# Kernel tuning notes

Hardware: AMD Instinct MI355X
Metric: run time of the kernel (lower is better)

## Reference

```python
import jax, jax.numpy as jnp
import numpy as np

HID = 128
HEADS = 4
N_LAYERS = 3


def layer_norm(x, g, b, eps=1e-5):
    mu = x.mean(-1, keepdims=True)
    var = ((x - mu) ** 2).mean(-1, keepdims=True)
    return (x - mu) / jnp.sqrt(var + eps) * g + b


def gat_layer(x, W, a_src, a_dst, bias, src, dst):
    # PyG GATConv(hidden, hidden, heads=4, concat=False): mean over heads, +bias
    N = x.shape[0]
    z = (x @ W).reshape(N, HEADS, HID)          # [N, H, D]
    e_src = (z * a_src[None]).sum(-1)           # [N, H]
    e_dst = (z * a_dst[None]).sum(-1)           # [N, H]
    e = jax.nn.leaky_relu(e_src[src] + e_dst[dst], 0.2)  # [E, H]
    m = jax.ops.segment_max(e, dst, num_segments=N)
    p = jnp.exp(e - m[dst])
    s = jax.ops.segment_sum(p, dst, num_segments=N)
    w = p / s[dst]                              # softmax over incoming edges
    out = jax.ops.segment_sum(w[:, :, None] * z[src], dst, num_segments=N)
    return out.mean(1) + bias                   # [N, D]


def _forward(x, node_W, node_b, gat_W, att_src, att_dst, gat_b, ln_g, ln_b,
             sW1, sb1, sW2, sb2, sW3, sb3, edge_index, odd_vertices):
    N = x.shape[0]
    loops = jnp.arange(N)                       # GATConv adds self-loops
    src = jnp.concatenate([edge_index[0], loops])
    dst = jnp.concatenate([edge_index[1], loops])
    h = jax.nn.relu(x @ node_W + node_b)
    for l in range(N_LAYERS):
        hn = gat_layer(h, gat_W[l], att_src[l], att_dst[l], gat_b[l], src, dst)
        hn = layer_norm(hn, ln_g[l], ln_b[l])
        h = jax.nn.relu(hn) + h                 # residual; dropout is eval-mode identity
    emb = h[odd_vertices]                       # [n_odd, D]
    n_odd = emb.shape[0]
    pair = jnp.concatenate([
        jnp.broadcast_to(emb[:, None, :], (n_odd, n_odd, HID)),
        jnp.broadcast_to(emb[None, :, :], (n_odd, n_odd, HID)),
    ], axis=-1)                                 # [n_odd, n_odd, 2D]
    t = jax.nn.relu(pair @ sW1 + sb1)
    t = jax.nn.relu(t @ sW2 + sb2)
    s = (t @ sW3 + sb3)[..., 0]                 # [n_odd, n_odd]
    U = jnp.triu(s, 1)                          # torch fills i<j then mirrors; diag 0
    return U + U.T


def setup_inputs() -> dict:
    key = jax.random.key(0)
    ks = jax.random.split(key, 12)
    N, E, F_IN, N_ODD = 20000, 320000, 5, 512
    sc = 0.05
    inp = {}
    inp["x"] = jax.random.normal(ks[0], (N, F_IN), jnp.float32)
    inp["edge_index"] = jax.random.randint(ks[1], (2, E), 0, N)
    inp["odd_vertices"] = jax.random.randint(ks[2], (N_ODD,), 0, N)
    inp["node_W"] = jax.random.normal(ks[3], (F_IN, HID), jnp.float32) * sc
    inp["node_b"] = jnp.zeros((HID,), jnp.float32)
    inp["gat_W"] = jax.random.normal(ks[4], (N_LAYERS, HID, HEADS * HID), jnp.float32) * sc
    inp["att_src"] = jax.random.normal(ks[5], (N_LAYERS, HEADS, HID), jnp.float32) * sc
    inp["att_dst"] = jax.random.normal(ks[6], (N_LAYERS, HEADS, HID), jnp.float32) * sc
    inp["gat_b"] = jnp.zeros((N_LAYERS, HID), jnp.float32)
    inp["ln_g"] = jnp.ones((N_LAYERS, HID), jnp.float32)
    inp["ln_b"] = jnp.zeros((N_LAYERS, HID), jnp.float32)
    inp["sW1"] = jax.random.normal(ks[7], (2 * HID, HID), jnp.float32) * sc
    inp["sb1"] = jnp.zeros((HID,), jnp.float32)
    inp["sW2"] = jax.random.normal(ks[8], (HID, HID), jnp.float32) * sc
    inp["sb2"] = jnp.zeros((HID,), jnp.float32)
    inp["sW3"] = jax.random.normal(ks[9], (HID, 1), jnp.float32) * sc
    inp["sb3"] = jnp.zeros((1,), jnp.float32)
    return inp


def reference(x, node_W, node_b, gat_W, att_src, att_dst, gat_b, ln_g, ln_b,
              sW1, sb1, sW2, sb2, sW3, sb3, edge_index, odd_vertices):
    return _forward(x, node_W, node_b, gat_W, att_src, att_dst, gat_b, ln_g, ln_b,
                    sW1, sb1, sW2, sb2, sW3, sb3, edge_index, odd_vertices)
```

## Files before the change

kernel.cpp:

```cpp
#include <hip/hip_runtime.h>

#define HID 128
#define HEADS 4
#define NODES 20000
#define NEDGE 320000
#define NTOT (NEDGE + NODES)
#define NODD 512

__global__ void hist_kernel(const int* __restrict__ ei, int* __restrict__ cnt) {
  int e = blockIdx.x * blockDim.x + threadIdx.x;
  if (e >= NTOT) return;
  int d = (e < NEDGE) ? ei[NEDGE + e] : (e - NEDGE);
  atomicAdd(&cnt[d], 1);
}

__global__ void scan_kernel(const int* __restrict__ cnt, int* __restrict__ row_start,
                            int* __restrict__ pos) {
  __shared__ int wsum[16];
  __shared__ int s_carry;
  int t = threadIdx.x;
  int lane = t & 63, wid = t >> 6;
  if (t == 0) s_carry = 0;
  __syncthreads();
  const int4* cnt4 = (const int4*)cnt;
  for (int base4 = 0; base4 < NODES / 4; base4 += 1024) {
    int idx4 = base4 + t;
    int4 v = {0, 0, 0, 0};
    if (idx4 < NODES / 4) v = cnt4[idx4];
    int s0 = v.x, s1 = s0 + v.y, s2 = s1 + v.z, s3 = s2 + v.w;
    int x = s3;
    for (int off = 1; off < 64; off <<= 1) {
      int y = __shfl_up(x, off, 64);
      if (lane >= off) x += y;
    }
    if (lane == 63) wsum[wid] = x;
    __syncthreads();
    if (wid == 0) {
      int w = (lane < 16) ? wsum[lane] : 0;
      for (int off = 1; off < 16; off <<= 1) {
        int y = __shfl_up(w, off, 64);
        if (lane >= off) w += y;
      }
      if (lane < 16) wsum[lane] = w;
    }
    __syncthreads();
    int waveoff = (wid == 0) ? 0 : wsum[wid - 1];
    int incl = s_carry + waveoff + x;
    int excl = incl - s3;
    if (idx4 < NODES / 4) {
      int o = idx4 * 4;
      row_start[o] = excl;          pos[o] = excl;
      row_start[o + 1] = excl + s0; pos[o + 1] = excl + s0;
      row_start[o + 2] = excl + s1; pos[o + 2] = excl + s1;
      row_start[o + 3] = excl + s2; pos[o + 3] = excl + s2;
    }
    __syncthreads();
    if (t == 1023) s_carry = incl;
    __syncthreads();
  }
  if (t == 0) row_start[NODES] = s_carry;
}

__global__ void scatter_kernel(const int* __restrict__ ei, int* __restrict__ pos,
                               int* __restrict__ csr_src) {
  int e = blockIdx.x * blockDim.x + threadIdx.x;
  if (e >= NTOT) return;
  int s, d;
  if (e < NEDGE) { s = ei[e]; d = ei[NEDGE + e]; } else { s = e - NEDGE; d = s; }
  int p = atomicAdd(&pos[d], 1);
  csr_src[p] = s;
}

__global__ void node_enc_kernel(const float* __restrict__ x, const float* __restrict__ W,
                                const float* __restrict__ b, float* __restrict__ h) {
  int idx = blockIdx.x * blockDim.x + threadIdx.x;
  if (idx >= NODES * HID) return;
  int n = idx >> 7, d = idx & 127;
  const float* xr = x + n * 5;
  float acc = b[d];
#pragma unroll
  for (int k = 0; k < 5; k++) acc = fmaf(xr[k], W[k * HID + d], acc);
  h[idx] = fmaxf(acc, 0.f);
}

__global__ void att_c_kernel(const float* __restrict__ W, const float* __restrict__ a_src,
                             const float* __restrict__ a_dst, float* __restrict__ c_src,
                             float* __restrict__ c_dst) {
  int h = blockIdx.x;
  int k = threadIdx.x;
  const float* wr = W + k * (HEADS * HID) + h * HID;
  const float* as = a_src + h * HID;
  const float* ad = a_dst + h * HID;
  float s1 = 0.f, s2 = 0.f;
  for (int d = 0; d < HID; d++) {
    float w = wr[d];
    s1 = fmaf(w, as[d], s1);
    s2 = fmaf(w, ad[d], s2);
  }
  c_src[h * HID + k] = s1;
  c_dst[h * HID + k] = s2;
}

__global__ __launch_bounds__(256) void e_kernel(const float* __restrict__ h,
    const float* __restrict__ c_src, const float* __restrict__ c_dst,
    float* __restrict__ e_src, float* __restrict__ e_dst) {
  int lane = threadIdx.x & 63;
  int wid = threadIdx.x >> 6;
  int n = blockIdx.x * 4 + wid;
  float v0 = h[n * HID + lane];
  float v1 = h[n * HID + 64 + lane];
#pragma unroll
  for (int hh = 0; hh < HEADS; hh++) {
    float p = v0 * c_src[hh * HID + lane] + v1 * c_src[hh * HID + 64 + lane];
#pragma unroll
    for (int m = 32; m; m >>= 1) p += __shfl_xor(p, m, 64);
    if (lane == 0) e_src[n * HEADS + hh] = p;
    float q = v0 * c_dst[hh * HID + lane] + v1 * c_dst[hh * HID + 64 + lane];
#pragma unroll
    for (int m = 32; m; m >>= 1) q += __shfl_xor(q, m, 64);
    if (lane == 0) e_dst[n * HEADS + hh] = q;
  }
}

__global__ __launch_bounds__(256) void agg_kernel(const float* __restrict__ h,
    const float* __restrict__ e_src, const float* __restrict__ e_dst,
    const int* __restrict__ row_start, const int* __restrict__ csr_src,
    float* __restrict__ agg, const int* __restrict__ map) {
  __shared__ float4 wsh[4][128];
  __shared__ int ssh[4][128];
  int lane = threadIdx.x & 63;
  int wid = threadIdx.x >> 6;
  int idx = blockIdx.x * 4 + wid;
  int n = map ? map[idx] : idx;
  int r0 = row_start[n], r1 = row_start[n + 1];
  int deg = r1 - r0;
  const float4* es4 = (const float4*)e_src;
  float4 ed = ((const float4*)e_dst)[n];

  int s0 = -1, s1 = -1;
  float4 v0 = {-1e30f, -1e30f, -1e30f, -1e30f};
  float4 v1 = {-1e30f, -1e30f, -1e30f, -1e30f};
  {
    int e = r0 + lane;
    if (e < r1) {
      s0 = csr_src[e];
      float4 es = es4[s0];
      float a = es.x + ed.x, b = es.y + ed.y, c = es.z + ed.z, d = es.w + ed.w;
      v0.x = a > 0.f ? a : 0.2f * a; v0.y = b > 0.f ? b : 0.2f * b;
      v0.z = c > 0.f ? c : 0.2f * c; v0.w = d > 0.f ? d : 0.2f * d;
    }
    e = r0 + 64 + lane;
    if (e < r1) {
      s1 = csr_src[e];
      float4 es = es4[s1];
      float a = es.x + ed.x, b = es.y + ed.y, c = es.z + ed.z, d = es.w + ed.w;
      v1.x = a > 0.f ? a : 0.2f * a; v1.y = b > 0.f ? b : 0.2f * b;
      v1.z = c > 0.f ? c : 0.2f * c; v1.w = d > 0.f ? d : 0.2f * d;
    }
  }
  float4 mx;
  mx.x = fmaxf(v0.x, v1.x); mx.y = fmaxf(v0.y, v1.y);
  mx.z = fmaxf(v0.z, v1.z); mx.w = fmaxf(v0.w, v1.w);
  for (int e = r0 + 128 + lane; e < r1; e += 64) {
    int s = csr_src[e];
    float4 es = es4[s];
    float a = es.x + ed.x, b = es.y + ed.y, c = es.z + ed.z, d = es.w + ed.w;
    mx.x = fmaxf(mx.x, a > 0.f ? a : 0.2f * a);
    mx.y = fmaxf(mx.y, b > 0.f ? b : 0.2f * b);
    mx.z = fmaxf(mx.z, c > 0.f ? c : 0.2f * c);
    mx.w = fmaxf(mx.w, d > 0.f ? d : 0.2f * d);
  }
#pragma unroll
  for (int m = 32; m; m >>= 1) {
    mx.x = fmaxf(mx.x, __shfl_xor(mx.x, m, 64));
    mx.y = fmaxf(mx.y, __shfl_xor(mx.y, m, 64));
    mx.z = fmaxf(mx.z, __shfl_xor(mx.z, m, 64));
    mx.w = fmaxf(mx.w, __shfl_xor(mx.w, m, 64));
  }
  float4 p0 = {0.f, 0.f, 0.f, 0.f}, p1 = {0.f, 0.f, 0.f, 0.f};
  if (s0 >= 0) { p0.x = expf(v0.x - mx.x); p0.y = expf(v0.y - mx.y);
                 p0.z = expf(v0.z - mx.z); p0.w = expf(v0.w - mx.w); }
  if (s1 >= 0) { p1.x = expf(v1.x - mx.x); p1.y = expf(v1.y - mx.y);
                 p1.z = expf(v1.z - mx.z); p1.w = expf(v1.w - mx.w); }
  float4 sm;
  sm.x = p0.x + p1.x; sm.y = p0.y + p1.y; sm.z = p0.z + p1.z; sm.w = p0.w + p1.w;
  for (int e = r0 + 128 + lane; e < r1; e += 64) {
    int s = csr_src[e];
    float4 es = es4[s];
    float a = es.x + ed.x, b = es.y + ed.y, c = es.z + ed.z, d = es.w + ed.w;
    a = a > 0.f ? a : 0.2f * a; b = b > 0.f ? b : 0.2f * b;
    c = c > 0.f ? c : 0.2f * c; d = d > 0.f ? d : 0.2f * d;
    sm.x += expf(a - mx.x); sm.y += expf(b - mx.y);
    sm.z += expf(c - mx.z); sm.w += expf(d - mx.w);
  }
#pragma unroll
  for (int m = 32; m; m >>= 1) {
    sm.x += __shfl_xor(sm.x, m, 64);
    sm.y += __shfl_xor(sm.y, m, 64);
    sm.z += __shfl_xor(sm.z, m, 64);
    sm.w += __shfl_xor(sm.w, m, 64);
  }
  float4 inv;
  inv.x = 1.f / sm.x; inv.y = 1.f / sm.y; inv.z = 1.f / sm.z; inv.w = 1.f / sm.w;

  if (s0 >= 0) {
    float4 w; w.x = p0.x * inv.x; w.y = p0.y * inv.y; w.z = p0.z * inv.z; w.w = p0.w * inv.w;
    wsh[wid][lane] = w; ssh[wid][lane] = s0;
  }
  if (s1 >= 0) {
    float4 w; w.x = p1.x * inv.x; w.y = p1.y * inv.y; w.z = p1.z * inv.z; w.w = p1.w * inv.w;
    wsh[wid][64 + lane] = w; ssh[wid][64 + lane] = s1;
  }
  __builtin_amdgcn_s_waitcnt(0);

  float2 a0 = {0.f, 0.f}, a1 = {0.f, 0.f}, a2 = {0.f, 0.f}, a3 = {0.f, 0.f};
  float2 b0 = {0.f, 0.f}, b1 = {0.f, 0.f}, b2 = {0.f, 0.f}, b3 = {0.f, 0.f};
  int mcap = deg < 128 ? deg : 128;
  int i = 0;
  for (; i + 2 <= mcap; i += 2) {
    float4 wA = wsh[wid][i];     int sA = ssh[wid][i];
    float4 wB = wsh[wid][i + 1]; int sB = ssh[wid][i + 1];
    float2 hA = ((const float2*)(h + sA * HID))[lane];
    float2 hB = ((const float2*)(h + sB * HID))[lane];
    a0.x = fmaf(wA.x, hA.x, a0.x); a0.y = fmaf(wA.x, hA.y, a0.y);
    a1.x = fmaf(wA.y, hA.x, a1.x); a1.y = fmaf(wA.y, hA.y, a1.y);
    a2.x = fmaf(wA.z, hA.x, a2.x); a2.y = fmaf(wA.z, hA.y, a2.y);
    a3.x = fmaf(wA.w, hA.x, a3.x); a3.y = fmaf(wA.w, hA.y, a3.y);
    b0.x = fmaf(wB.x, hB.x, b0.x); b0.y = fmaf(wB.x, hB.y, b0.y);
    b1.x = fmaf(wB.y, hB.x, b1.x); b1.y = fmaf(wB.y, hB.y, b1.y);
    b2.x = fmaf(wB.z, hB.x, b2.x); b2.y = fmaf(wB.z, hB.y, b2.y);
    b3.x = fmaf(wB.w, hB.x, b3.x); b3.y = fmaf(wB.w, hB.y, b3.y);
  }
  if (i < mcap) {
    float4 w = wsh[wid][i];
    int s = ssh[wid][i];
    float2 hv = ((const float2*)(h + s * HID))[lane];
    a0.x = fmaf(w.x, hv.x, a0.x); a0.y = fmaf(w.x, hv.y, a0.y);
    a1.x = fmaf(w.y, hv.x, a1.x); a1.y = fmaf(w.y, hv.y, a1.y);
    a2.x = fmaf(w.z, hv.x, a2.x); a2.y = fmaf(w.z, hv.y, a2.y);
    a3.x = fmaf(w.w, hv.x, a3.x); a3.y = fmaf(w.w, hv.y, a3.y);
  }
  a0.x += b0.x; a0.y += b0.y; a1.x += b1.x; a1.y += b1.y;
  a2.x += b2.x; a2.y += b2.y; a3.x += b3.x; a3.y += b3.y;
  for (int e = r0 + 128; e < r1; e++) {
    int s = csr_src[e];
    float4 es = es4[s];
    float a = es.x + ed.x, b = es.y + ed.y, c = es.z + ed.z, d = es.w + ed.w;
    a = a > 0.f ? a : 0.2f * a; b = b > 0.f ? b : 0.2f * b;
    c = c > 0.f ? c : 0.2f * c; d = d > 0.f ? d : 0.2f * d;
    float w0 = expf(a - mx.x) * inv.x, w1 = expf(b - mx.y) * inv.y;
    float w2 = expf(c - mx.z) * inv.z, w3 = expf(d - mx.w) * inv.w;
    float2 hv = ((const float2*)(h + s * HID))[lane];
    a0.x = fmaf(w0, hv.x, a0.x); a0.y = fmaf(w0, hv.y, a0.y);
    a1.x = fmaf(w1, hv.x, a1.x); a1.y = fmaf(w1, hv.y, a1.y);
    a2.x = fmaf(w2, hv.x, a2.x); a2.y = fmaf(w2, hv.y, a2.y);
    a3.x = fmaf(w3, hv.x, a3.x); a3.y = fmaf(w3, hv.y, a3.y);
  }
  float* ap = agg + idx * 512;
  ((float2*)(ap + 0 * 128))[lane] = a0;
  ((float2*)(ap + 1 * 128))[lane] = a1;
  ((float2*)(ap + 2 * 128))[lane] = a2;
  ((float2*)(ap + 3 * 128))[lane] = a3;
}

__global__ __launch_bounds__(256) void out_ln_kernel(const float* __restrict__ agg,
    const float* __restrict__ W, const float* __restrict__ bias,
    const float* __restrict__ g, const float* __restrict__ b,
    const float* __restrict__ h_in, float* __restrict__ h_out,
    const int* __restrict__ map) {
  __shared__ float As[32][36];
  __shared__ float Bs[32][132];
  int tid = threadIdx.x;
  int nb = blockIdx.x * 32;
  int tdim = tid & 31;
  int tnode = tid >> 5;
  float acc[4][4] = {};
  for (int kb = 0; kb < 512; kb += 32) {
    int hh = kb >> 7;
    int kk0 = kb & 127;
    __syncthreads();
    {
      int n = tid >> 3, kq = tid & 7;
      float4 v = *(const float4*)(agg + (nb + n) * 512 + kb + kq * 4);
      As[kq * 4 + 0][n] = v.x; As[kq * 4 + 1][n] = v.y;
      As[kq * 4 + 2][n] = v.z; As[kq * 4 + 3][n] = v.w;
#pragma unroll
      for (int i = 0; i < 4; i++) {
        int idx4 = tid + i * 256;
        int r = idx4 >> 5, dq = idx4 & 31;
        float4 w = *(const float4*)(W + (kk0 + r) * 512 + hh * 128 + dq * 4);
        *(float4*)&Bs[r][dq * 4] = w;
      }
    }
    __syncthreads();
#pragma unroll
    for (int k = 0; k < 32; k++) {
      float4 av = *(const float4*)&As[k][tnode * 4];
      float4 bv = *(const float4*)&Bs[k][tdim * 4];
      acc[0][0] = fmaf(av.x, bv.x, acc[0][0]); acc[0][1] = fmaf(av.x, bv.y, acc[0][1]);
      acc[0][2] = fmaf(av.x, bv.z, acc[0][2]); acc[0][3] = fmaf(av.x, bv.w, acc[0][3]);
      acc[1][0] = fmaf(av.y, bv.x, acc[1][0]); acc[1][1] = fmaf(av.y, bv.y, acc[1][1]);
      acc[1][2] = fmaf(av.y, bv.z, acc[1][2]); acc[1][3] = fmaf(av.y, bv.w, acc[1][3]);
      acc[2][0] = fmaf(av.z, bv.x, acc[2][0]); acc[2][1] = fmaf(av.z, bv.y, acc[2][1]);
      acc[2][2] = fmaf(av.z, bv.z, acc[2][2]); acc[2][3] = fmaf(av.z, bv.w, acc[2][3]);
      acc[3][0] = fmaf(av.w, bv.x, acc[3][0]); acc[3][1] = fmaf(av.w, bv.y, acc[3][1]);
      acc[3][2] = fmaf(av.w, bv.z, acc[3][2]); acc[3][3] = fmaf(av.w, bv.w, acc[3][3]);
    }
  }
  float4 bias4 = *(const float4*)(bias + tdim * 4);
  float4 g4 = *(const float4*)(g + tdim * 4);
  float4 b4 = *(const float4*)(b + tdim * 4);
#pragma unroll
  for (int i = 0; i < 4; i++) {
    int row = nb + tnode * 4 + i;
    int res = map ? map[row] : row;
    float o0 = acc[i][0] * 0.25f + bias4.x;
    float o1 = acc[i][1] * 0.25f + bias4.y;
    float o2 = acc[i][2] * 0.25f + bias4.z;
    float o3 = acc[i][3] * 0.25f + bias4.w;
    float s1 = o0 + o1 + o2 + o3;
    float s2 = o0 * o0 + o1 * o1 + o2 * o2 + o3 * o3;
#pragma unroll
    for (int m = 1; m < 32; m <<= 1) {
      s1 += __shfl_xor(s1, m, 64);
      s2 += __shfl_xor(s2, m, 64);
    }
    float mu = s1 * 0.0078125f;
    float var = s2 * 0.0078125f - mu * mu;
    float r = 1.0f / sqrtf(var + 1e-5f);
    float4 hi = *(const float4*)(h_in + res * 128 + tdim * 4);
    float4 o;
    o.x = fmaxf((o0 - mu) * r * g4.x + b4.x, 0.f) + hi.x;
    o.y = fmaxf((o1 - mu) * r * g4.y + b4.y, 0.f) + hi.y;
    o.z = fmaxf((o2 - mu) * r * g4.z + b4.z, 0.f) + hi.z;
    o.w = fmaxf((o3 - mu) * r * g4.w + b4.w, 0.f) + hi.w;
    *(float4*)(h_out + row * 128 + tdim * 4) = o;
  }
}

__global__ __launch_bounds__(128) void ab_kernel(const float* __restrict__ emb,
    const float* __restrict__ sW1, const float* __restrict__ sb1,
    float* __restrict__ As, float* __restrict__ Bs) {
  __shared__ float se[HID];
  int i = blockIdx.x;
  int k = threadIdx.x;
  se[k] = emb[i * HID + k];
  __syncthreads();
  float a = sb1[k], b = 0.f;
  for (int d = 0; d < HID; d++) {
    float e = se[d];
    a = fmaf(e, sW1[d * HID + k], a);
    b = fmaf(e, sW1[(HID + d) * HID + k], b);
  }
  As[i * HID + k] = a;
  Bs[i * HID + k] = b;
}

__global__ __launch_bounds__(256) void score_kernel(const float* __restrict__ As,
    const float* __restrict__ Bs, const float* __restrict__ sW2,
    const float* __restrict__ sb2, const float* __restrict__ sW3,
    const float* __restrict__ sb3, float* __restrict__ out) {
  int bx = blockIdx.x, by = blockIdx.y;
  if (bx > by) return;
  int i0 = bx * 8, j0 = by * 8;
  __shared__ float T1[32][68];
  __shared__ float W2s[32][132];
  int tid = threadIdx.x;
  int tn = tid & 15;
  int tp = tid >> 4;
  int sp = tid >> 2;
  int kq = (tid & 3) * 8;
  const float* arow = As + (i0 + (sp >> 3)) * 128;
  const float* brow = Bs + (j0 + (sp & 7)) * 128;
  float acc[4][8] = {};
  for (int kb = 0; kb < 128; kb += 32) {
    __syncthreads();
    {
      float4 a0 = *(const float4*)(arow + kb + kq);
      float4 b0 = *(const float4*)(brow + kb + kq);
      float4 a1 = *(const float4*)(arow + kb + kq + 4);
      float4 b1 = *(const float4*)(brow + kb + kq + 4);
      T1[kq + 0][sp] = fmaxf(a0.x + b0.x, 0.f);
      T1[kq + 1][sp] = fmaxf(a0.y + b0.y, 0.f);
      T1[kq + 2][sp] = fmaxf(a0.z + b0.z, 0.f);
      T1[kq + 3][sp] = fmaxf(a0.w + b0.w, 0.f);
      T1[kq + 4][sp] = fmaxf(a1.x + b1.x, 0.f);
      T1[kq + 5][sp] = fmaxf(a1.y + b1.y, 0.f);
      T1[kq + 6][sp] = fmaxf(a1.z + b1.z, 0.f);
      T1[kq + 7][sp] = fmaxf(a1.w + b1.w, 0.f);
#pragma unroll
      for (int i = 0; i < 4; i++) {
        int idx4 = tid + i * 256;
        int r = idx4 >> 5, c = (idx4 & 31) * 4;
        float4 w = *(const float4*)(sW2 + (kb + r) * 128 + c);
        *(float4*)&W2s[r][c] = w;
      }
    }
    __syncthreads();
#pragma unroll
    for (int k = 0; k < 32; k++) {
      float4 av  = *(const float4*)&T1[k][tp * 4];
      float4 bv0 = *(const float4*)&W2s[k][tn * 4];
      float4 bv1 = *(const float4*)&W2s[k][64 + tn * 4];
#pragma unroll
      for (int p = 0; p < 4; p++) {
        float a = (p == 0) ? av.x : (p == 1) ? av.y : (p == 2) ? av.z : av.w;
        acc[p][0] = fmaf(a, bv0.x, acc[p][0]); acc[p][1] = fmaf(a, bv0.y, acc[p][1]);
        acc[p][2] = fmaf(a, bv0.z, acc[p][2]); acc[p][3] = fmaf(a, bv0.w, acc[p][3]);
        acc[p][4] = fmaf(a, bv1.x, acc[p][4]); acc[p][5] = fmaf(a, bv1.y, acc[p][5]);
        acc[p][6] = fmaf(a, bv1.z, acc[p][6]); acc[p][7] = fmaf(a, bv1.w, acc[p][7]);
      }
    }
  }
  float4 b2a = *(const float4*)(sb2 + tn * 4);
  float4 b2b = *(const float4*)(sb2 + 64 + tn * 4);
  float4 w3a = *(const float4*)(sW3 + tn * 4);
  float4 w3b = *(const float4*)(sW3 + 64 + tn * 4);
  float b3v = sb3[0];
#pragma unroll
  for (int pr = 0; pr < 4; pr++) {
    float s = fmaxf(acc[pr][0] + b2a.x, 0.f) * w3a.x
            + fmaxf(acc[pr][1] + b2a.y, 0.f) * w3a.y
            + fmaxf(acc[pr][2] + b2a.z, 0.f) * w3a.z
            + fmaxf(acc[pr][3] + b2a.w, 0.f) * w3a.w
            + fmaxf(acc[pr][4] + b2b.x, 0.f) * w3b.x
            + fmaxf(acc[pr][5] + b2b.y, 0.f) * w3b.y
            + fmaxf(acc[pr][6] + b2b.z, 0.f) * w3b.z
            + fmaxf(acc[pr][7] + b2b.w, 0.f) * w3b.w;
#pragma unroll
    for (int m = 1; m < 16; m <<= 1) s += __shfl_xor(s, m, 64);
    if (tn == 0) {
      int p = tp * 4 + pr;
      int i = i0 + (p >> 3), j = j0 + (p & 7);
      if (i < j) {
        float v = s + b3v;
        out[i * 512 + j] = v;
        out[j * 512 + i] = v;
      } else if (i == j) {
        out[i * 512 + j] = 0.f;
      }
    }
  }
}

extern "C" void kernel_launch(void* const* d_in, const int* in_sizes, int n_in,
                              void* d_out, int out_size, void* d_ws, size_t ws_size,
                              hipStream_t stream) {
  const float* x       = (const float*)d_in[0];
  const int*   ei      = (const int*)d_in[1];
  const int*   odd     = (const int*)d_in[2];
  const float* node_W  = (const float*)d_in[3];
  const float* node_b  = (const float*)d_in[4];
  const float* gat_W   = (const float*)d_in[5];
  const float* att_src = (const float*)d_in[6];
  const float* att_dst = (const float*)d_in[7];
  const float* gat_b   = (const float*)d_in[8];
  const float* ln_g    = (const float*)d_in[9];
  const float* ln_b    = (const float*)d_in[10];
  const float* sW1     = (const float*)d_in[11];
  const float* sb1     = (const float*)d_in[12];
  const float* sW2     = (const float*)d_in[13];
  const float* sb2     = (const float*)d_in[14];
  const float* sW3     = (const float*)d_in[15];
  const float* sb3     = (const float*)d_in[16];
  float* out = (float*)d_out;

  float* f = (float*)d_ws;
  float* hA  = f; f += NODES * HID;
  float* hB  = f; f += NODES * HID;
  float* agg = f; f += NODES * 512;
  float* e_s = f; f += NODES * 4;
  float* e_d = f; f += NODES * 4;
  float* c_s = f; f += 512;
  float* c_d = f; f += 512;
  float* Asb = f; f += NODD * HID;
  float* Bsb = f; f += NODD * HID;
  float* emb = f; f += NODD * HID;
  int* cnt       = (int*)f;
  int* row_start = cnt + NODES;
  int* pos       = row_start + NODES + 1;
  int* csr       = pos + NODES;

  hipMemsetAsync(cnt, 0, NODES * sizeof(int), stream);
  hist_kernel<<<(NTOT + 255) / 256, 256, 0, stream>>>(ei, cnt);
  scan_kernel<<<1, 1024, 0, stream>>>(cnt, row_start, pos);
  scatter_kernel<<<(NTOT + 255) / 256, 256, 0, stream>>>(ei, pos, csr);
  node_enc_kernel<<<(NODES * HID + 255) / 256, 256, 0, stream>>>(x, node_W, node_b, hA);

  const float* hc = hA;
  float* hn = hB;
  for (int l = 0; l < 2; l++) {
    att_c_kernel<<<HEADS, 128, 0, stream>>>(gat_W + l * HID * 512,
                                            att_src + l * 512, att_dst + l * 512, c_s, c_d);
    e_kernel<<<NODES / 4, 256, 0, stream>>>(hc, c_s, c_d, e_s, e_d);
    agg_kernel<<<NODES / 4, 256, 0, stream>>>(hc, e_s, e_d, row_start, csr, agg, nullptr);
    out_ln_kernel<<<NODES / 32, 256, 0, stream>>>(agg, gat_W + l * HID * 512,
                                                  gat_b + l * HID, ln_g + l * HID,
                                                  ln_b + l * HID, hc, hn, nullptr);
    float* t = (float*)hc; hc = hn; hn = t;
  }
  {
    const int l = 2;
    att_c_kernel<<<HEADS, 128, 0, stream>>>(gat_W + l * HID * 512,
                                            att_src + l * 512, att_dst + l * 512, c_s, c_d);
    e_kernel<<<NODES / 4, 256, 0, stream>>>(hc, c_s, c_d, e_s, e_d);
    agg_kernel<<<NODD / 4, 256, 0, stream>>>(hc, e_s, e_d, row_start, csr, agg, odd);
    out_ln_kernel<<<NODD / 32, 256, 0, stream>>>(agg, gat_W + l * HID * 512,
                                                 gat_b + l * HID, ln_g + l * HID,
                                                 ln_b + l * HID, hc, emb, odd);
  }
  ab_kernel<<<NODD, 128, 0, stream>>>(emb, sW1, sb1, Asb, Bsb);
  score_kernel<<<dim3(64, 64), 256, 0, stream>>>(Asb, Bsb, sW2, sb2, sW3, sb3, out);
}
```

Before: 458.1 us.

## Fuse attention-logit computation into node encoder and LayerNorm epilogue

```diff
diff --git a/kernel.cpp b/kernel.cpp
--- a/kernel.cpp
+++ b/kernel.cpp
@@ -71,54 +71,61 @@
   csr_src[p] = s;
 }
 
-__global__ void node_enc_kernel(const float* __restrict__ x, const float* __restrict__ W,
-                                const float* __restrict__ b, float* __restrict__ h) {
-  int idx = blockIdx.x * blockDim.x + threadIdx.x;
-  if (idx >= NODES * HID) return;
-  int n = idx >> 7, d = idx & 127;
-  const float* xr = x + n * 5;
-  float acc = b[d];
-#pragma unroll
-  for (int k = 0; k < 5; k++) acc = fmaf(xr[k], W[k * HID + d], acc);
-  h[idx] = fmaxf(acc, 0.f);
-}
-
-__global__ void att_c_kernel(const float* __restrict__ W, const float* __restrict__ a_src,
-                             const float* __restrict__ a_dst, float* __restrict__ c_src,
-                             float* __restrict__ c_dst) {
-  int h = blockIdx.x;
+__global__ void att_c_all_kernel(const float* __restrict__ gat_W,
+                                 const float* __restrict__ a_src,
+                                 const float* __restrict__ a_dst,
+                                 float* __restrict__ c_src, float* __restrict__ c_dst) {
+  int l = blockIdx.x >> 2;
+  int h = blockIdx.x & 3;
   int k = threadIdx.x;
-  const float* wr = W + k * (HEADS * HID) + h * HID;
-  const float* as = a_src + h * HID;
-  const float* ad = a_dst + h * HID;
+  const float* wr = gat_W + l * HID * 512 + k * 512 + h * HID;
+  const float* as = a_src + l * 512 + h * HID;
+  const float* ad = a_dst + l * 512 + h * HID;
   float s1 = 0.f, s2 = 0.f;
   for (int d = 0; d < HID; d++) {
     float w = wr[d];
     s1 = fmaf(w, as[d], s1);
     s2 = fmaf(w, ad[d], s2);
   }
-  c_src[h * HID + k] = s1;
-  c_dst[h * HID + k] = s2;
-}
-
-__global__ __launch_bounds__(256) void e_kernel(const float* __restrict__ h,
-    const float* __restrict__ c_src, const float* __restrict__ c_dst,
-    float* __restrict__ e_src, float* __restrict__ e_dst) {
+  c_src[l * 512 + h * HID + k] = s1;
+  c_dst[l * 512 + h * HID + k] = s2;
+}
+
+__global__ __launch_bounds__(256) void node_enc_e_kernel(const float* __restrict__ x,
+    const float* __restrict__ W, const float* __restrict__ b,
+    const float* __restrict__ cs, const float* __restrict__ cd,
+    float* __restrict__ h, float* __restrict__ e_s, float* __restrict__ e_d) {
   int lane = threadIdx.x & 63;
   int wid = threadIdx.x >> 6;
   int n = blockIdx.x * 4 + wid;
-  float v0 = h[n * HID + lane];
-  float v1 = h[n * HID + 64 + lane];
+  const float* xr = x + n * 5;
+  float x0 = xr[0], x1 = xr[1], x2 = xr[2], x3 = xr[3], x4 = xr[4];
+  int d0 = lane * 2;
+  float2 bb = *(const float2*)(b + d0);
+  float h0 = bb.x, h1 = bb.y;
+  {
+    float2 w;
+    w = *(const float2*)(W + 0 * HID + d0); h0 = fmaf(x0, w.x, h0); h1 = fmaf(x0, w.y, h1);
+    w = *(const float2*)(W + 1 * HID + d0); h0 = fmaf(x1, w.x, h0); h1 = fmaf(x1, w.y, h1);
+    w = *(const float2*)(W + 2 * HID + d0); h0 = fmaf(x2, w.x, h0); h1 = fmaf(x2, w.y, h1);
+    w = *(const float2*)(W + 3 * HID + d0); h0 = fmaf(x3, w.x, h0); h1 = fmaf(x3, w.y, h1);
+    w = *(const float2*)(W + 4 * HID + d0); h0 = fmaf(x4, w.x, h0); h1 = fmaf(x4, w.y, h1);
+  }
+  h0 = fmaxf(h0, 0.f); h1 = fmaxf(h1, 0.f);
+  float2 hv = {h0, h1};
+  ((float2*)(h + n * HID))[lane] = hv;
 #pragma unroll
   for (int hh = 0; hh < HEADS; hh++) {
-    float p = v0 * c_src[hh * HID + lane] + v1 * c_src[hh * HID + 64 + lane];
-#pragma unroll
-    for (int m = 32; m; m >>= 1) p += __shfl_xor(p, m, 64);
-    if (lane == 0) e_src[n * HEADS + hh] = p;
-    float q = v0 * c_dst[hh * HID + lane] + v1 * c_dst[hh * HID + 64 + lane];
-#pragma unroll
-    for (int m = 32; m; m >>= 1) q += __shfl_xor(q, m, 64);
-    if (lane == 0) e_dst[n * HEADS + hh] = q;
+    float2 c1 = *(const float2*)(cs + hh * HID + d0);
+    float2 c2 = *(const float2*)(cd + hh * HID + d0);
+    float p = h0 * c1.x + h1 * c1.y;
+    float q = h0 * c2.x + h1 * c2.y;
+#pragma unroll
+    for (int m = 32; m; m >>= 1) {
+      p += __shfl_xor(p, m, 64);
+      q += __shfl_xor(q, m, 64);
+    }
+    if (lane == 0) { e_s[n * HEADS + hh] = p; e_d[n * HEADS + hh] = q; }
   }
 }
 
@@ -267,7 +274,9 @@
     const float* __restrict__ W, const float* __restrict__ bias,
     const float* __restrict__ g, const float* __restrict__ b,
     const float* __restrict__ h_in, float* __restrict__ h_out,
-    const int* __restrict__ map) {
+    const int* __restrict__ map,
+    const float* __restrict__ cs_next, const float* __restrict__ cd_next,
+    float* __restrict__ e_s_out, float* __restrict__ e_d_out) {
   __shared__ float As[32][36];
   __shared__ float Bs[32][132];
   int tid = threadIdx.x;
@@ -310,6 +319,14 @@
   float4 bias4 = *(const float4*)(bias + tdim * 4);
   float4 g4 = *(const float4*)(g + tdim * 4);
   float4 b4 = *(const float4*)(b + tdim * 4);
+  float4 cs4[4], cd4[4];
+  if (cs_next) {
+#pragma unroll
+    for (int hh = 0; hh < 4; hh++) {
+      cs4[hh] = *(const float4*)(cs_next + hh * 128 + tdim * 4);
+      cd4[hh] = *(const float4*)(cd_next + hh * 128 + tdim * 4);
+    }
+  }
 #pragma unroll
   for (int i = 0; i < 4; i++) {
     int row = nb + tnode * 4 + i;
@@ -335,6 +352,22 @@
     o.z = fmaxf((o2 - mu) * r * g4.z + b4.z, 0.f) + hi.z;
     o.w = fmaxf((o3 - mu) * r * g4.w + b4.w, 0.f) + hi.w;
     *(float4*)(h_out + row * 128 + tdim * 4) = o;
+    if (cs_next) {
+#pragma unroll
+      for (int hh = 0; hh < 4; hh++) {
+        float ps = o.x * cs4[hh].x + o.y * cs4[hh].y + o.z * cs4[hh].z + o.w * cs4[hh].w;
+        float pd = o.x * cd4[hh].x + o.y * cd4[hh].y + o.z * cd4[hh].z + o.w * cd4[hh].w;
+#pragma unroll
+        for (int m = 1; m < 32; m <<= 1) {
+          ps += __shfl_xor(ps, m, 64);
+          pd += __shfl_xor(pd, m, 64);
+        }
+        if (tdim == 0) {
+          e_s_out[row * 4 + hh] = ps;
+          e_d_out[row * 4 + hh] = pd;
+        }
+      }
+    }
   }
 }
 
@@ -471,8 +504,8 @@
   float* agg = f; f += NODES * 512;
   float* e_s = f; f += NODES * 4;
   float* e_d = f; f += NODES * 4;
-  float* c_s = f; f += 512;
-  float* c_d = f; f += 512;
+  float* c_s = f; f += 3 * 512;
+  float* c_d = f; f += 3 * 512;
   float* Asb = f; f += NODD * HID;
   float* Bsb = f; f += NODD * HID;
   float* emb = f; f += NODD * HID;
@@ -485,29 +518,28 @@
   hist_kernel<<<(NTOT + 255) / 256, 256, 0, stream>>>(ei, cnt);
   scan_kernel<<<1, 1024, 0, stream>>>(cnt, row_start, pos);
   scatter_kernel<<<(NTOT + 255) / 256, 256, 0, stream>>>(ei, pos, csr);
-  node_enc_kernel<<<(NODES * HID + 255) / 256, 256, 0, stream>>>(x, node_W, node_b, hA);
+  att_c_all_kernel<<<12, 128, 0, stream>>>(gat_W, att_src, att_dst, c_s, c_d);
+  node_enc_e_kernel<<<NODES / 4, 256, 0, stream>>>(x, node_W, node_b,
+                                                   c_s, c_d, hA, e_s, e_d);
 
   const float* hc = hA;
   float* hn = hB;
   for (int l = 0; l < 2; l++) {
-    att_c_kernel<<<HEADS, 128, 0, stream>>>(gat_W + l * HID * 512,
-                                            att_src + l * 512, att_dst + l * 512, c_s, c_d);
-    e_kernel<<<NODES / 4, 256, 0, stream>>>(hc, c_s, c_d, e_s, e_d);
     agg_kernel<<<NODES / 4, 256, 0, stream>>>(hc, e_s, e_d, row_start, csr, agg, nullptr);
     out_ln_kernel<<<NODES / 32, 256, 0, stream>>>(agg, gat_W + l * HID * 512,
                                                   gat_b + l * HID, ln_g + l * HID,
-                                                  ln_b + l * HID, hc, hn, nullptr);
+                                                  ln_b + l * HID, hc, hn, nullptr,
+                                                  c_s + (l + 1) * 512, c_d + (l + 1) * 512,
+                                                  e_s, e_d);
     float* t = (float*)hc; hc = hn; hn = t;
   }
   {
     const int l = 2;
-    att_c_kernel<<<HEADS, 128, 0, stream>>>(gat_W + l * HID * 512,
-                                            att_src + l * 512, att_dst + l * 512, c_s, c_d);
-    e_kernel<<<NODES / 4, 256, 0, stream>>>(hc, c_s, c_d, e_s, e_d);
     agg_kernel<<<NODD / 4, 256, 0, stream>>>(hc, e_s, e_d, row_start, csr, agg, odd);
     out_ln_kernel<<<NODD / 32, 256, 0, stream>>>(agg, gat_W + l * HID * 512,
                                                  gat_b + l * HID, ln_g + l * HID,
-                                                 ln_b + l * HID, hc, emb, odd);
+                                                 ln_b + l * HID, hc, emb, odd,
+                                                 nullptr, nullptr, nullptr, nullptr);
   }
   ab_kernel<<<NODD, 128, 0, stream>>>(emb, sW1, sb1, Asb, Bsb);
   score_kernel<<<dim3(64, 64), 256, 0, stream>>>(Asb, Bsb, sW2, sb2, sW3, sb3, out);
```

After: 426.5 us. -6.9%, faster.
